# Optimization experiments

Measured on AMD Instinct MI355X. Metric: run time of the kernel, lower is better.

## Reference

```python
import jax, jax.numpy as jnp
import numpy as np

B, N, D = 8, 2048, 512

def setup_inputs() -> dict:
    key = jax.random.key(0)
    k1, k2, k3, k4 = jax.random.split(key, 4)
    x = jax.random.normal(k1, (B, N, D), dtype=jnp.float32)
    x2 = jax.random.normal(k2, (B, N, D), dtype=jnp.float32)
    # nn.Linear(dim, dim): weight [D, D], bias [D]
    W = jax.random.normal(k3, (D, D), dtype=jnp.float32) * (1.0 / np.sqrt(D))
    b = jax.random.normal(k4, (D,), dtype=jnp.float32) * 0.01
    return {"x": x, "x2": x2, "W": W, "b": b}

def reference(x, x2, W, b):
    # key = softmax(x2.transpose(1,2), dim=1) -> softmax over feature axis D,
    # shape [B, D, N]; equivalently softmax(x2, axis=-1) then transpose.
    key_t = jax.nn.softmax(x2, axis=-1)          # [B, N, D], softmax over D
    query = jax.nn.softmax(x2, axis=1)            # [B, N, D], softmax over N
    # context = value @ key : [B,N,D] @ [B,D,N] -> [B,N,N]
    context = jnp.einsum('bnd,bmd->bnm', x, key_t)
    # atten = context @ query : [B,N,N] @ [B,N,D] -> [B,N,D]
    atten = jnp.einsum('bnm,bmd->bnd', context, query)
    # linear projection: atten @ W.T + b
    return jnp.einsum('bnd,ed->bne', atten, W) + b
```

## Files before the change

### kernel.cpp

```cpp
#include <hip/hip_runtime.h>


typedef __attribute__((ext_vector_type(8))) short          s16x8;
typedef __attribute__((ext_vector_type(8))) unsigned short u16x8;
typedef __attribute__((ext_vector_type(4))) float          f32x4;

#define B_ 8
#define N_ 2048
#define D_ 512

__device__ inline unsigned short f2bf(float f) {
    unsigned u = __float_as_uint(f);
    u += 0x7FFFu + ((u >> 16) & 1u);
    return (unsigned short)(u >> 16);
}

__global__ __launch_bounds__(256) void fused_sums_k(const float* __restrict__ x2,
                                                    float* __restrict__ rsq,
                                                    float* __restrict__ qs) {
    __shared__ float cp[4][512];
    int w = threadIdx.x >> 6, l = threadIdx.x & 63;
    int rbase = blockIdx.x * 32;
    int b = rbase / N_;
    const int c0 = l * 8;
    float colacc[8] = {0.f, 0.f, 0.f, 0.f, 0.f, 0.f, 0.f, 0.f};
#pragma unroll
    for (int rr = 0; rr < 8; ++rr) {
        int r = rbase + w * 8 + rr;
        const float* p = x2 + (size_t)r * D_ + c0;
        float4 a = *(const float4*)p;
        float4 bb = *(const float4*)(p + 4);
        float e0 = __expf(a.x), e1 = __expf(a.y), e2 = __expf(a.z), e3 = __expf(a.w);
        float e4 = __expf(bb.x), e5 = __expf(bb.y), e6 = __expf(bb.z), e7 = __expf(bb.w);
        float s = e0 + e1 + e2 + e3 + e4 + e5 + e6 + e7;
#pragma unroll
        for (int off = 1; off < 64; off <<= 1) s += __shfl_xor(s, off);
        if (l == 0) rsq[r] = sqrtf(1.0f / s);
        colacc[0] += e0; colacc[1] += e1; colacc[2] += e2; colacc[3] += e3;
        colacc[4] += e4; colacc[5] += e5; colacc[6] += e6; colacc[7] += e7;
    }
#pragma unroll
    for (int c = 0; c < 8; ++c) cp[w][c0 + c] = colacc[c];
    __syncthreads();
    for (int c = threadIdx.x; c < 512; c += 256) {
        float s = cp[0][c] + cp[1][c] + cp[2][c] + cp[3][c];
        atomicAdd(&qs[b * D_ + c], s);
    }
}

__global__ __launch_bounds__(256) void softmax_ft_k(const float* __restrict__ x2,
                                                    const float* __restrict__ rsq,
                                                    unsigned short* __restrict__ Ft) {
    __shared__ unsigned short ft[64][65];
    int b  = 7 - blockIdx.z;
    int d0 = (7 - blockIdx.y) * 64;
    int m0 = (31 - blockIdx.x) * 64;
    int tx = threadIdx.x & 63, w = threadIdx.x >> 6;
#pragma unroll
    for (int it = 0; it < 16; ++it) {
        int row = w * 16 + it;
        float v = x2[((size_t)b * N_ + m0 + row) * D_ + d0 + tx];
        float sc = rsq[b * N_ + m0 + row];
        ft[tx][row] = f2bf(__expf(v) * sc);
    }
    __syncthreads();
#pragma unroll
    for (int it = 0; it < 16; ++it) {
        int dr = w * 16 + it;
        Ft[((size_t)b * D_ + d0 + dr) * N_ + m0 + tx] = ft[dr][tx];
    }
}

__global__ __launch_bounds__(256) void cvt_bf16_k(const float* __restrict__ in,
                                                  unsigned short* __restrict__ out) {
    size_t i = ((size_t)blockIdx.x * 256 + threadIdx.x) * 8;
    float4 a = *(const float4*)(in + i);
    float4 b = *(const float4*)(in + i + 4);
    u16x8 o;
    o[0] = f2bf(a.x); o[1] = f2bf(a.y); o[2] = f2bf(a.z); o[3] = f2bf(a.w);
    o[4] = f2bf(b.x); o[5] = f2bf(b.y); o[6] = f2bf(b.z); o[7] = f2bf(b.w);
    *(u16x8*)(out + i) = o;
}

__global__ __launch_bounds__(256) void cvt_kq_k(const float* __restrict__ P,
                                                const float* __restrict__ qs,
                                                unsigned short* __restrict__ KQb) {
    size_t o = ((size_t)blockIdx.x * 256 + threadIdx.x) * 8;
    int b = (int)(o >> 18);
    size_t off = o & 262143;
    int j0 = (int)(o & 511);
    const float* p0 = P + ((size_t)b * 2) * 262144 + off;
    const float* p1 = p0 + 262144;
    float4 a0 = *(const float4*)p0,        a1 = *(const float4*)(p0 + 4);
    float4 c0 = *(const float4*)p1,        c1 = *(const float4*)(p1 + 4);
    float4 q0 = *(const float4*)(qs + b * D_ + j0);
    float4 q1 = *(const float4*)(qs + b * D_ + j0 + 4);
    u16x8 r;
    r[0] = f2bf((a0.x + c0.x) / q0.x); r[1] = f2bf((a0.y + c0.y) / q0.y);
    r[2] = f2bf((a0.z + c0.z) / q0.z); r[3] = f2bf((a0.w + c0.w) / q0.w);
    r[4] = f2bf((a1.x + c1.x) / q1.x); r[5] = f2bf((a1.y + c1.y) / q1.y);
    r[6] = f2bf((a1.z + c1.z) / q1.z); r[7] = f2bf((a1.w + c1.w) / q1.w);
    *(u16x8*)(KQb + o) = r;
}

__device__ inline void gload16(const unsigned short* g, unsigned short* l) {
    __builtin_amdgcn_global_load_lds((const __attribute__((address_space(1))) void*)g,
                                     (__attribute__((address_space(3))) void*)l, 16, 0, 0);
}
__device__ inline void gload16f(const float* g, float* l) {
    __builtin_amdgcn_global_load_lds((const __attribute__((address_space(1))) void*)g,
                                     (__attribute__((address_space(3))) void*)l, 16, 0, 0);
}

template <int MODE>
__global__ __launch_bounds__(256, 4) void gemm64_k(const unsigned short* __restrict__ A,
                                                   const unsigned short* __restrict__ Bm,
                                                   void* __restrict__ Cv,
                                                   int M, int N, int K, int nsplit,
                                                   long long sA, long long sB, long long sC) {
    __shared__ unsigned short As[64 * 32], Bs[64 * 32];
    int b = blockIdx.z / nsplit, ks = blockIdx.z % nsplit;
    int klen = K / nsplit, k0 = ks * klen;
    const unsigned short* Ab = A + (size_t)b * sA;
    const unsigned short* Bb = Bm + (size_t)b * sB;
    int tid = threadIdx.x, w = tid >> 6, l = tid & 63;
    int wr = w >> 1, wc = w & 1;
    int lr = l & 15, lg = l >> 4;
    int srow = tid >> 2, scc = tid & 3;

    f32x4 acc[2][2];
#pragma unroll
    for (int i = 0; i < 2; ++i)
#pragma unroll
        for (int j = 0; j < 2; ++j) acc[i][j] = (f32x4){0.f, 0.f, 0.f, 0.f};

    const int rowbase = blockIdx.y * 64, colbase = blockIdx.x * 64;

    for (int kt = k0; kt < k0 + klen; kt += 32) {
        gload16(Ab + (size_t)(rowbase + srow) * K + kt + scc * 8, As + w * 512);
        gload16(Bb + (size_t)(colbase + srow) * K + kt + scc * 8, Bs + w * 512);
        __syncthreads();
        s16x8 af[2], bf[2];
#pragma unroll
        for (int i = 0; i < 2; ++i)
            af[i] = *(const s16x8*)&As[(wr * 32 + i * 16 + lr) * 32 + lg * 8];
#pragma unroll
        for (int j = 0; j < 2; ++j)
            bf[j] = *(const s16x8*)&Bs[(wc * 32 + j * 16 + lr) * 32 + lg * 8];
#pragma unroll
        for (int i = 0; i < 2; ++i)
#pragma unroll
            for (int j = 0; j < 2; ++j)
                acc[i][j] = __builtin_amdgcn_mfma_f32_16x16x32_bf16(af[i], bf[j], acc[i][j], 0, 0, 0);
        __syncthreads();
    }

    if (MODE == 0) {
        float* C = (float*)Cv + (size_t)blockIdx.z * sC;
#pragma unroll
        for (int i = 0; i < 2; ++i)
#pragma unroll
            for (int j = 0; j < 2; ++j) {
                int col = colbase + wc * 32 + j * 16 + lr;
#pragma unroll
                for (int r = 0; r < 4; ++r) {
                    int row = rowbase + wr * 32 + i * 16 + lg * 4 + r;
                    C[(size_t)row * N + col] = acc[i][j][r];
                }
            }
    } else {
        unsigned short* C = (unsigned short*)Cv + (size_t)b * sC;
#pragma unroll
        for (int i = 0; i < 2; ++i)
#pragma unroll
            for (int j = 0; j < 2; ++j) {
                int col = colbase + wc * 32 + j * 16 + lr;
#pragma unroll
                for (int r = 0; r < 4; ++r) {
                    int row = rowbase + wr * 32 + i * 16 + lg * 4 + r;
                    C[(size_t)row * N + col] = f2bf(acc[i][j][r]);
                }
            }
    }
}

__global__ __launch_bounds__(256, 2) void gemm_xf32_k(const float* __restrict__ X,
                                                      const unsigned short* __restrict__ Bm,
                                                      float* __restrict__ Out,
                                                      const float* __restrict__ bias) {
    __shared__ float Asf[128 * 32];
    __shared__ unsigned short Bs[128 * 32];
    int b = blockIdx.z;
    const float* Ab = X + (size_t)b * ((size_t)N_ * D_);
    const unsigned short* Bb = Bm + (size_t)b * ((size_t)D_ * D_);
    int tm = blockIdx.y, tn = blockIdx.x;
    int tid = threadIdx.x, w = tid >> 6, l = tid & 63;
    int wr = w >> 1, wc = w & 1;
    int lr = l & 15, lg = l >> 4;

    f32x4 acc[4][4];
#pragma unroll
    for (int i = 0; i < 4; ++i)
#pragma unroll
        for (int j = 0; j < 4; ++j) acc[i][j] = (f32x4){0.f, 0.f, 0.f, 0.f};

    const int rowbase = tm * 128, colbase = tn * 128;

    for (int kt = 0; kt < D_; kt += 32) {
#pragma unroll
        for (int i = 0; i < 4; ++i) {
            int ci = (i * 4 + w) * 64 + l;
            int row = ci >> 3, cc = ci & 7;
            gload16f(Ab + (size_t)(rowbase + row) * D_ + kt + cc * 4, Asf + (i * 4 + w) * 256);
        }
#pragma unroll
        for (int i = 0; i < 2; ++i) {
            int ci = (i * 4 + w) * 64 + l;
            int row = ci >> 2, cc = ci & 3;
            gload16(Bb + (size_t)(colbase + row) * D_ + kt + cc * 8, Bs + (i * 4 + w) * 512);
        }
        __syncthreads();
        s16x8 af[4], bf[4];
#pragma unroll
        for (int i = 0; i < 4; ++i) {
            const float* ap = &Asf[(wr * 64 + i * 16 + lr) * 32 + lg * 8];
            f32x4 a0 = *(const f32x4*)ap, a1 = *(const f32x4*)(ap + 4);
            s16x8 t;
            t[0] = (short)f2bf(a0[0]); t[1] = (short)f2bf(a0[1]);
            t[2] = (short)f2bf(a0[2]); t[3] = (short)f2bf(a0[3]);
            t[4] = (short)f2bf(a1[0]); t[5] = (short)f2bf(a1[1]);
            t[6] = (short)f2bf(a1[2]); t[7] = (short)f2bf(a1[3]);
            af[i] = t;
        }
#pragma unroll
        for (int j = 0; j < 4; ++j)
            bf[j] = *(const s16x8*)&Bs[(wc * 64 + j * 16 + lr) * 32 + lg * 8];
#pragma unroll
        for (int i = 0; i < 4; ++i)
#pragma unroll
            for (int j = 0; j < 4; ++j)
                acc[i][j] = __builtin_amdgcn_mfma_f32_16x16x32_bf16(af[i], bf[j], acc[i][j], 0, 0, 0);
        __syncthreads();
    }

    float* C = Out + (size_t)b * ((size_t)N_ * D_);
#pragma unroll
    for (int i = 0; i < 4; ++i)
#pragma unroll
        for (int j = 0; j < 4; ++j) {
            int col = colbase + wc * 64 + j * 16 + lr;
            float bv = bias[col];
#pragma unroll
            for (int r = 0; r < 4; ++r) {
                int row = rowbase + wr * 64 + i * 16 + lg * 4 + r;
                C[(size_t)row * D_ + col] = acc[i][j][r] + bv;
            }
        }
}

extern "C" void kernel_launch(void* const* d_in, const int* in_sizes, int n_in,
                              void* d_out, int out_size, void* d_ws, size_t ws_size,
                              hipStream_t stream) {
    const float* x    = (const float*)d_in[0];
    const float* x2   = (const float*)d_in[1];
    const float* W    = (const float*)d_in[2];
    const float* bias = (const float*)d_in[3];
    float* out = (float*)d_out;

    unsigned short* Ft  = (unsigned short*)d_ws;
    unsigned short* Wb  = Ft + 8388608;
    unsigned short* KQb = Wb + 262144;
    unsigned short* Mt  = KQb + 2097152;
    float* P   = (float*)(Mt + 2097152);
    float* qs  = P + 4194304;
    float* rsq = qs + 4096;

    hipMemsetAsync(qs, 0, (size_t)B_ * D_ * sizeof(float), stream);

    fused_sums_k<<<dim3(B_ * N_ / 32), 256, 0, stream>>>(x2, rsq, qs);

    softmax_ft_k<<<dim3(N_ / 64, D_ / 64, B_), 256, 0, stream>>>(x2, rsq, Ft);

    cvt_bf16_k<<<dim3(128), 256, 0, stream>>>(W, Wb);

    gemm64_k<0><<<dim3(8, 8, B_ * 2), 256, 0, stream>>>(
        Ft, Ft, P, 512, 512, 2048, 2,
        (long long)512 * 2048, (long long)512 * 2048, (long long)512 * 512);

    cvt_kq_k<<<dim3(1024), 256, 0, stream>>>(P, qs, KQb);

    gemm64_k<2><<<dim3(8, 8, B_), 256, 0, stream>>>(
        Wb, KQb, Mt, 512, 512, 512, 1,
        0LL, (long long)512 * 512, (long long)512 * 512);

    gemm_xf32_k<<<dim3(4, 16, B_), 256, 0, stream>>>(x, Mt, out, bias);
}
```

Before: 183.1 us.

## Fuse softmax passes into one kernel and use 128-tile split-4 Gram GEMM

Merges the row-sum kernel and the transposing softmax kernel into a single kernel. It normalizes each row in registers, stages the tile in LDS and writes the transposed bf16 F directly, so x2 is read only once. The Ft·Ftᵀ GEMM moves from 64x64 tiles with split-K 2 to a dedicated 128x128 tile kernel with split-K 4. That gives more reuse per tile, but doubles the fp32 partial buffer that the reduction kernel now sums over four slices. The large LDS tile in the fused kernel may lower occupancy, and its transposed reads may hit LDS bank conflicts.

```diff
diff --git a/kernel.cpp b/kernel.cpp
--- a/kernel.cpp
+++ b/kernel.cpp
@@ -15,19 +15,19 @@
     return (unsigned short)(u >> 16);
 }
 
-__global__ __launch_bounds__(256) void fused_sums_k(const float* __restrict__ x2,
-                                                    float* __restrict__ rsq,
-                                                    float* __restrict__ qs) {
+__global__ __launch_bounds__(256) void softmax_fused_k(const float* __restrict__ x2,
+                                                       unsigned short* __restrict__ Ft,
+                                                       float* __restrict__ qs) {
+    __shared__ unsigned short ft[64][522];
     __shared__ float cp[4][512];
+    int b = blockIdx.y, m0 = blockIdx.x * 64;
     int w = threadIdx.x >> 6, l = threadIdx.x & 63;
-    int rbase = blockIdx.x * 32;
-    int b = rbase / N_;
     const int c0 = l * 8;
     float colacc[8] = {0.f, 0.f, 0.f, 0.f, 0.f, 0.f, 0.f, 0.f};
 #pragma unroll
-    for (int rr = 0; rr < 8; ++rr) {
-        int r = rbase + w * 8 + rr;
-        const float* p = x2 + (size_t)r * D_ + c0;
+    for (int it = 0; it < 16; ++it) {
+        int row = w * 16 + it;
+        const float* p = x2 + ((size_t)b * N_ + m0 + row) * D_ + c0;
         float4 a = *(const float4*)p;
         float4 bb = *(const float4*)(p + 4);
         float e0 = __expf(a.x), e1 = __expf(a.y), e2 = __expf(a.z), e3 = __expf(a.w);
@@ -35,7 +35,11 @@
         float s = e0 + e1 + e2 + e3 + e4 + e5 + e6 + e7;
 #pragma unroll
         for (int off = 1; off < 64; off <<= 1) s += __shfl_xor(s, off);
-        if (l == 0) rsq[r] = sqrtf(1.0f / s);
+        float rv = rsqrtf(s);
+        u16x8 o;
+        o[0] = f2bf(e0 * rv); o[1] = f2bf(e1 * rv); o[2] = f2bf(e2 * rv); o[3] = f2bf(e3 * rv);
+        o[4] = f2bf(e4 * rv); o[5] = f2bf(e5 * rv); o[6] = f2bf(e6 * rv); o[7] = f2bf(e7 * rv);
+        *(u16x8*)&ft[row][c0] = o;
         colacc[0] += e0; colacc[1] += e1; colacc[2] += e2; colacc[3] += e3;
         colacc[4] += e4; colacc[5] += e5; colacc[6] += e6; colacc[7] += e7;
     }
@@ -46,28 +50,17 @@
         float s = cp[0][c] + cp[1][c] + cp[2][c] + cp[3][c];
         atomicAdd(&qs[b * D_ + c], s);
     }
-}
-
-__global__ __launch_bounds__(256) void softmax_ft_k(const float* __restrict__ x2,
-                                                    const float* __restrict__ rsq,
-                                                    unsigned short* __restrict__ Ft) {
-    __shared__ unsigned short ft[64][65];
-    int b  = 7 - blockIdx.z;
-    int d0 = (7 - blockIdx.y) * 64;
-    int m0 = (31 - blockIdx.x) * 64;
-    int tx = threadIdx.x & 63, w = threadIdx.x >> 6;
-#pragma unroll
-    for (int it = 0; it < 16; ++it) {
-        int row = w * 16 + it;
-        float v = x2[((size_t)b * N_ + m0 + row) * D_ + d0 + tx];
-        float sc = rsq[b * N_ + m0 + row];
-        ft[tx][row] = f2bf(__expf(v) * sc);
-    }
-    __syncthreads();
-#pragma unroll
-    for (int it = 0; it < 16; ++it) {
-        int dr = w * 16 + it;
-        Ft[((size_t)b * D_ + d0 + dr) * N_ + m0 + tx] = ft[dr][tx];
+#pragma unroll
+    for (int half = 0; half < 2; ++half) {
+        int d = threadIdx.x + half * 256;
+        unsigned short* dst = Ft + ((size_t)b * D_ + d) * N_ + m0;
+#pragma unroll
+        for (int mv = 0; mv < 8; ++mv) {
+            u16x8 o;
+#pragma unroll
+            for (int k = 0; k < 8; ++k) o[k] = ft[mv * 8 + k][d];
+            *(u16x8*)(dst + mv * 8) = o;
+        }
     }
 }
 
@@ -89,17 +82,22 @@
     int b = (int)(o >> 18);
     size_t off = o & 262143;
     int j0 = (int)(o & 511);
-    const float* p0 = P + ((size_t)b * 2) * 262144 + off;
-    const float* p1 = p0 + 262144;
-    float4 a0 = *(const float4*)p0,        a1 = *(const float4*)(p0 + 4);
-    float4 c0 = *(const float4*)p1,        c1 = *(const float4*)(p1 + 4);
+    const float* base = P + (size_t)b * 4 * 262144 + off;
+    float4 s0 = {0.f, 0.f, 0.f, 0.f}, s1 = {0.f, 0.f, 0.f, 0.f};
+#pragma unroll
+    for (int s = 0; s < 4; ++s) {
+        float4 a0 = *(const float4*)(base + (size_t)s * 262144);
+        float4 a1 = *(const float4*)(base + (size_t)s * 262144 + 4);
+        s0.x += a0.x; s0.y += a0.y; s0.z += a0.z; s0.w += a0.w;
+        s1.x += a1.x; s1.y += a1.y; s1.z += a1.z; s1.w += a1.w;
+    }
     float4 q0 = *(const float4*)(qs + b * D_ + j0);
     float4 q1 = *(const float4*)(qs + b * D_ + j0 + 4);
     u16x8 r;
-    r[0] = f2bf((a0.x + c0.x) / q0.x); r[1] = f2bf((a0.y + c0.y) / q0.y);
-    r[2] = f2bf((a0.z + c0.z) / q0.z); r[3] = f2bf((a0.w + c0.w) / q0.w);
-    r[4] = f2bf((a1.x + c1.x) / q1.x); r[5] = f2bf((a1.y + c1.y) / q1.y);
-    r[6] = f2bf((a1.z + c1.z) / q1.z); r[7] = f2bf((a1.w + c1.w) / q1.w);
+    r[0] = f2bf(s0.x / q0.x); r[1] = f2bf(s0.y / q0.y);
+    r[2] = f2bf(s0.z / q0.z); r[3] = f2bf(s0.w / q0.w);
+    r[4] = f2bf(s1.x / q1.x); r[5] = f2bf(s1.y / q1.y);
+    r[6] = f2bf(s1.z / q1.z); r[7] = f2bf(s1.w / q1.w);
     *(u16x8*)(KQb + o) = r;
 }
 
@@ -112,15 +110,69 @@
                                      (__attribute__((address_space(3))) void*)l, 16, 0, 0);
 }
 
-template <int MODE>
+__global__ __launch_bounds__(256, 2) void gemm128_p2_k(const unsigned short* __restrict__ Ft,
+                                                       float* __restrict__ P) {
+    __shared__ unsigned short As[128 * 32], Bs[128 * 32];
+    const int nsplit = 4, K = N_;
+    int z = blockIdx.z, b = z >> 2, ks = z & 3;
+    int klen = K / nsplit, k0 = ks * klen;
+    const unsigned short* Ab = Ft + (size_t)b * ((size_t)D_ * N_);
+    int tid = threadIdx.x, w = tid >> 6, l = tid & 63;
+    int wr = w >> 1, wc = w & 1;
+    int lr = l & 15, lg = l >> 4;
+
+    f32x4 acc[4][4];
+#pragma unroll
+    for (int i = 0; i < 4; ++i)
+#pragma unroll
+        for (int j = 0; j < 4; ++j) acc[i][j] = (f32x4){0.f, 0.f, 0.f, 0.f};
+
+    const int rowbase = blockIdx.y * 128, colbase = blockIdx.x * 128;
+
+    for (int kt = k0; kt < k0 + klen; kt += 32) {
+#pragma unroll
+        for (int i = 0; i < 2; ++i) {
+            int ci = (i * 4 + w) * 64 + l;
+            int row = ci >> 2, cc = ci & 3;
+            gload16(Ab + (size_t)(rowbase + row) * K + kt + cc * 8, As + (i * 4 + w) * 512);
+            gload16(Ab + (size_t)(colbase + row) * K + kt + cc * 8, Bs + (i * 4 + w) * 512);
+        }
+        __syncthreads();
+        s16x8 af[4], bf[4];
+#pragma unroll
+        for (int i = 0; i < 4; ++i)
+            af[i] = *(const s16x8*)&As[(wr * 64 + i * 16 + lr) * 32 + lg * 8];
+#pragma unroll
+        for (int j = 0; j < 4; ++j)
+            bf[j] = *(const s16x8*)&Bs[(wc * 64 + j * 16 + lr) * 32 + lg * 8];
+#pragma unroll
+        for (int i = 0; i < 4; ++i)
+#pragma unroll
+            for (int j = 0; j < 4; ++j)
+                acc[i][j] = __builtin_amdgcn_mfma_f32_16x16x32_bf16(af[i], bf[j], acc[i][j], 0, 0, 0);
+        __syncthreads();
+    }
+
+    float* C = P + (size_t)z * 262144;
+#pragma unroll
+    for (int i = 0; i < 4; ++i)
+#pragma unroll
+        for (int j = 0; j < 4; ++j) {
+            int col = colbase + wc * 64 + j * 16 + lr;
+#pragma unroll
+            for (int r = 0; r < 4; ++r) {
+                int row = rowbase + wr * 64 + i * 16 + lg * 4 + r;
+                C[(size_t)row * D_ + col] = acc[i][j][r];
+            }
+        }
+}
+
 __global__ __launch_bounds__(256, 4) void gemm64_k(const unsigned short* __restrict__ A,
                                                    const unsigned short* __restrict__ Bm,
-                                                   void* __restrict__ Cv,
-                                                   int M, int N, int K, int nsplit,
-                                                   long long sA, long long sB, long long sC) {
+                                                   unsigned short* __restrict__ Cv,
+                                                   int K, long long sA, long long sB, long long sC) {
     __shared__ unsigned short As[64 * 32], Bs[64 * 32];
-    int b = blockIdx.z / nsplit, ks = blockIdx.z % nsplit;
-    int klen = K / nsplit, k0 = ks * klen;
+    int b = blockIdx.z;
     const unsigned short* Ab = A + (size_t)b * sA;
     const unsigned short* Bb = Bm + (size_t)b * sB;
     int tid = threadIdx.x, w = tid >> 6, l = tid & 63;
@@ -136,7 +188,7 @@
 
     const int rowbase = blockIdx.y * 64, colbase = blockIdx.x * 64;
 
-    for (int kt = k0; kt < k0 + klen; kt += 32) {
+    for (int kt = 0; kt < K; kt += 32) {
         gload16(Ab + (size_t)(rowbase + srow) * K + kt + scc * 8, As + w * 512);
         gload16(Bb + (size_t)(colbase + srow) * K + kt + scc * 8, Bs + w * 512);
         __syncthreads();
@@ -155,33 +207,18 @@
         __syncthreads();
     }
 
-    if (MODE == 0) {
-        float* C = (float*)Cv + (size_t)blockIdx.z * sC;
-#pragma unroll
-        for (int i = 0; i < 2; ++i)
-#pragma unroll
-            for (int j = 0; j < 2; ++j) {
-                int col = colbase + wc * 32 + j * 16 + lr;
-#pragma unroll
-                for (int r = 0; r < 4; ++r) {
-                    int row = rowbase + wr * 32 + i * 16 + lg * 4 + r;
-                    C[(size_t)row * N + col] = acc[i][j][r];
-                }
+    unsigned short* C = Cv + (size_t)b * sC;
+#pragma unroll
+    for (int i = 0; i < 2; ++i)
+#pragma unroll
+        for (int j = 0; j < 2; ++j) {
+            int col = colbase + wc * 32 + j * 16 + lr;
+#pragma unroll
+            for (int r = 0; r < 4; ++r) {
+                int row = rowbase + wr * 32 + i * 16 + lg * 4 + r;
+                C[(size_t)row * D_ + col] = f2bf(acc[i][j][r]);
             }
-    } else {
-        unsigned short* C = (unsigned short*)Cv + (size_t)b * sC;
-#pragma unroll
-        for (int i = 0; i < 2; ++i)
-#pragma unroll
-            for (int j = 0; j < 2; ++j) {
-                int col = colbase + wc * 32 + j * 16 + lr;
-#pragma unroll
-                for (int r = 0; r < 4; ++r) {
-                    int row = rowbase + wr * 32 + i * 16 + lg * 4 + r;
-                    C[(size_t)row * N + col] = f2bf(acc[i][j][r]);
-                }
-            }
-    }
+        }
 }
 
 __global__ __launch_bounds__(256, 2) void gemm_xf32_k(const float* __restrict__ X,
@@ -272,26 +309,20 @@
     unsigned short* KQb = Wb + 262144;
     unsigned short* Mt  = KQb + 2097152;
     float* P   = (float*)(Mt + 2097152);
-    float* qs  = P + 4194304;
-    float* rsq = qs + 4096;
+    float* qs  = P + 8388608;
 
     hipMemsetAsync(qs, 0, (size_t)B_ * D_ * sizeof(float), stream);
 
-    fused_sums_k<<<dim3(B_ * N_ / 32), 256, 0, stream>>>(x2, rsq, qs);
-
-    softmax_ft_k<<<dim3(N_ / 64, D_ / 64, B_), 256, 0, stream>>>(x2, rsq, Ft);
+    softmax_fused_k<<<dim3(N_ / 64, B_), 256, 0, stream>>>(x2, Ft, qs);
 
     cvt_bf16_k<<<dim3(128), 256, 0, stream>>>(W, Wb);
 
-    gemm64_k<0><<<dim3(8, 8, B_ * 2), 256, 0, stream>>>(
-        Ft, Ft, P, 512, 512, 2048, 2,
-        (long long)512 * 2048, (long long)512 * 2048, (long long)512 * 512);
+    gemm128_p2_k<<<dim3(4, 4, B_ * 4), 256, 0, stream>>>(Ft, P);
 
     cvt_kq_k<<<dim3(1024), 256, 0, stream>>>(P, qs, KQb);
 
-    gemm64_k<2><<<dim3(8, 8, B_), 256, 0, stream>>>(
-        Wb, KQb, Mt, 512, 512, 512, 1,
-        0LL, (long long)512 * 512, (long long)512 * 512);
+    gemm64_k<<<dim3(8, 8, B_), 256, 0, stream>>>(
+        Wb, KQb, Mt, 512, 0LL, (long long)512 * 512, (long long)512 * 512);
 
     gemm_xf32_k<<<dim3(4, 16, B_), 256, 0, stream>>>(x, Mt, out, bias);
 }
```

Result: faster. 174.4 us (-4.7%).
